# Kernel tuning notes

Measured on AMD Instinct MI355X. Metric: run time of the kernel, lower is better.

The kernel has to match this reference:

```python
import jax, jax.numpy as jnp
import numpy as np

N = 50000   # nodes
E = 800000  # edges (before self loops)
V = 30000   # vocab
D = 128     # emb_dim == hidden_dim
G = 64      # graphs in batch
L = 2       # num_layers
NEG_SLOPE = 0.2
LN_EPS = 1e-5


def setup_inputs() -> dict:
    key = jax.random.key(0)
    ks = jax.random.split(key, 12)
    node_ids = jax.random.randint(ks[0], (N,), 0, V)
    edge_index = jax.random.randint(ks[1], (2, E), 0, N)
    edge_weight = jax.random.uniform(ks[2], (E,), dtype=jnp.float32)
    batch = jnp.sort(jax.random.randint(ks[3], (N,), 0, G))
    s = 0.05
    emb = (jax.random.normal(ks[4], (V, D), dtype=jnp.float32) * s).at[0].set(0.0)  # padding_idx=0
    ln_g = jnp.ones((L, D), jnp.float32)
    ln_b = jnp.zeros((L, D), jnp.float32)
    att_w = jax.random.normal(ks[5], (L, 2 * D), dtype=jnp.float32) * s  # Linear(2D,1,bias=False)
    w1 = jax.random.normal(ks[6], (L, D, D), dtype=jnp.float32) * s
    b1 = jnp.zeros((L, D), jnp.float32)
    w2 = jax.random.normal(ks[7], (L, D, D), dtype=jnp.float32) * s
    b2 = jnp.zeros((L, D), jnp.float32)
    eps = jnp.zeros((L,), jnp.float32)  # trainable eps, init 0
    wh1 = jax.random.normal(ks[8], (D, D // 2), dtype=jnp.float32) * s
    bh1 = jnp.zeros((D // 2,), jnp.float32)
    wh2 = jax.random.normal(ks[9], (D // 2, 2), dtype=jnp.float32) * s
    bh2 = jnp.zeros((2,), jnp.float32)
    return dict(node_ids=node_ids, edge_index=edge_index, edge_weight=edge_weight, batch=batch,
                emb=emb, ln_g=ln_g, ln_b=ln_b, att_w=att_w, w1=w1, b1=b1, w2=w2, b2=b2,
                eps=eps, wh1=wh1, bh1=bh1, wh2=wh2, bh2=bh2)


def _layer_norm(x, g, b):
    mu = jnp.mean(x, axis=-1, keepdims=True)
    var = jnp.mean(jnp.square(x - mu), axis=-1, keepdims=True)
    return (x - mu) * jax.lax.rsqrt(var + LN_EPS) * g + b


def _conv(x, src, dst, ew, aw, W1, B1, W2, B2, e):
    # attention score: cat([x_i, x_j]) @ aw  ==  x_i @ aw[:D] + x_j @ aw[D:]
    score = x[dst] @ aw[:D] + x[src] @ aw[D:]            # [E2]
    score = jnp.where(score >= 0, score, NEG_SLOPE * score)  # leaky_relu(0.2)
    smax = jax.ops.segment_max(score, dst, num_segments=N)   # per-target max (all nodes have self loop)
    ex = jnp.exp(score - smax[dst])
    denom = jax.ops.segment_sum(ex, dst, num_segments=N)
    alpha = ex / (denom[dst] + 1e-16)                    # segment softmax (PyG softmax)
    alpha = alpha * ew                                   # edge weights (dropout is identity at eval)
    agg = jax.ops.segment_sum(alpha[:, None] * x[src], dst, num_segments=N)  # scatter-add messages
    out = (1.0 + e) * x + agg                            # GIN update
    return jax.nn.relu(out @ W1 + B1) @ W2 + B2          # conv MLP


def reference(node_ids, edge_index, edge_weight, batch, emb, ln_g, ln_b, att_w,
              w1, b1, w2, b2, eps, wh1, bh1, wh2, bh2):
    x = emb[node_ids]                                    # [N, D]
    loop = jnp.arange(N, dtype=edge_index.dtype)
    src = jnp.concatenate([edge_index[0], loop])         # add_self_loops
    dst = jnp.concatenate([edge_index[1], loop])
    ew = jnp.concatenate([edge_weight, jnp.ones((N,), edge_weight.dtype)])
    for l in range(L):
        x = _layer_norm(x, ln_g[l], ln_b[l])
        x = _conv(x, src, dst, ew, att_w[l], w1[l], b1[l], w2[l], b2[l], eps[l])
        x = jax.nn.relu(x)
    # global_mean_pool
    ones = jnp.ones((N,), x.dtype)
    counts = jax.ops.segment_sum(ones, batch, num_segments=G)
    g = jax.ops.segment_sum(x, batch, num_segments=G) / jnp.maximum(counts, 1.0)[:, None]
    # head MLP -> [G, 2]
    return jax.nn.relu(g @ wh1 + bh1) @ wh2 + bh2
```

## Files before the change

kernel.cpp:

```cpp
#include <hip/hip_runtime.h>

#define NN 50000
#define NPAD 50048
#define DD 128
#define GG 64
#define NBLK 49

typedef __attribute__((ext_vector_type(8))) short short8;
typedef __attribute__((ext_vector_type(4))) float f32x4;

__device__ __forceinline__ unsigned short f2bf(float f){
  union { float f; unsigned u; } x; x.f = f;
  unsigned r = x.u + 0x7fffu + ((x.u >> 16) & 1u);
  return (unsigned short)(r >> 16);
}
__device__ __forceinline__ float bf2f(unsigned short h){
  union { unsigned u; float f; } x; x.u = ((unsigned)h) << 16;
  return x.f;
}
__device__ __forceinline__ f32x4 mfma16(short8 a, short8 b, f32x4 c){
  return __builtin_amdgcn_mfma_f32_16x16x32_bf16(a, b, c, 0, 0, 0);
}

__device__ __forceinline__ float wave_reduce_sum(float v){
  #pragma unroll
  for (int off = 32; off; off >>= 1) v += __shfl_xor(v, off, 64);
  return v;
}
__device__ __forceinline__ float wave_reduce_max(float v){
  #pragma unroll
  for (int off = 32; off; off >>= 1) v = fmaxf(v, __shfl_xor(v, off, 64));
  return v;
}

__global__ __launch_bounds__(256) void gather_kernel(const int* __restrict__ ids,
    const float* __restrict__ emb, float* __restrict__ x){
  int t = blockIdx.x * 256 + threadIdx.x;
  if (t >= NN * 32) return;
  int row = t >> 5, c = (t & 31) << 2;
  int id = ids[row];
  *(float4*)&x[(size_t)row * DD + c] = *(const float4*)&emb[(size_t)id * DD + c];
}

__global__ __launch_bounds__(256) void pack_w_kernel(const float* __restrict__ w1,
    const float* __restrict__ w2, short* __restrict__ wph, short* __restrict__ wpl){
  int i = blockIdx.x * 256 + threadIdx.x;
  int m = i >> 14, k = (i >> 7) & 127, c = i & 127;
  const float* src = (m & 1) ? w2 : w1;
  float v = src[((size_t)(m >> 1) * 128 + k) * 128 + c];
  unsigned short h = f2bf(v);
  float lo = v - bf2f(h);
  int idx = (m << 14) + ((k >> 3) << 10) + (c << 3) + (k & 7);
  wph[idx] = (short)h;
  wpl[idx] = (short)f2bf(lo);
}

__global__ __launch_bounds__(256) void count_kernel(const int* __restrict__ dst,
    int* __restrict__ cnt, int E){
  int e = blockIdx.x * 256 + threadIdx.x;
  if (e < E) atomicAdd(&cnt[dst[e]], 1);
}

__global__ __launch_bounds__(256) void scan1_kernel(const int* __restrict__ cnt,
    int* __restrict__ rp, int* __restrict__ bsum){
  __shared__ int wsum[4];
  int tid = threadIdx.x, lane = tid & 63, wid = tid >> 6;
  int base = blockIdx.x * 1024 + tid * 4;
  int4 v = {0,0,0,0};
  if (base < NN) v = *(const int4*)&cnt[base];
  int tsum = v.x + v.y + v.z + v.w;
  int incl = tsum;
  #pragma unroll
  for (int off = 1; off < 64; off <<= 1){
    int t = __shfl_up(incl, off, 64);
    if (lane >= off) incl += t;
  }
  if (lane == 63) wsum[wid] = incl;
  __syncthreads();
  int woff = 0;
  for (int w = 0; w < wid; ++w) woff += wsum[w];
  int excl = woff + incl - tsum;
  if (base < NN){
    int4 o;
    o.x = excl; o.y = excl + v.x; o.z = excl + v.x + v.y; o.w = excl + v.x + v.y + v.z;
    *(int4*)&rp[base] = o;
  }
  if (tid == 0) bsum[blockIdx.x] = wsum[0] + wsum[1] + wsum[2] + wsum[3];
}

__global__ __launch_bounds__(64) void scan2_kernel(int* __restrict__ bsum, int* __restrict__ rp){
  int lane = threadIdx.x;
  int v = (lane < NBLK) ? bsum[lane] : 0;
  int incl = v;
  #pragma unroll
  for (int off = 1; off < 64; off <<= 1){
    int t = __shfl_up(incl, off, 64);
    if (lane >= off) incl += t;
  }
  if (lane < NBLK) bsum[lane] = incl - v;
  if (lane == 63) rp[NN] = incl;
}

__global__ __launch_bounds__(256) void scan3_kernel(const int* __restrict__ bsum,
    int* __restrict__ rp, int* __restrict__ cursor){
  int base = blockIdx.x * 1024 + threadIdx.x * 4;
  if (base >= NN) return;
  int add = bsum[blockIdx.x];
  int4 t = *(const int4*)&rp[base];
  t.x += add; t.y += add; t.z += add; t.w += add;
  *(int4*)&rp[base] = t;
  *(int4*)&cursor[base] = t;
}

__global__ __launch_bounds__(256) void scatter_kernel(const int* __restrict__ src,
    const int* __restrict__ dst, const float* __restrict__ ew,
    int* __restrict__ cursor, int* __restrict__ csr_src, float* __restrict__ csr_ew, int E){
  int e = blockIdx.x * 256 + threadIdx.x;
  if (e >= E) return;
  int d = dst[e];
  int p = atomicAdd(&cursor[d], 1);
  csr_src[p] = src[e];
  csr_ew[p] = ew[e];
}

__global__ __launch_bounds__(256) void ln_kernel(float* __restrict__ x,
    const float* __restrict__ gamma, const float* __restrict__ beta,
    const float* __restrict__ aw,
    float* __restrict__ sd, float* __restrict__ ss, float* __restrict__ selfsc){
  int n = (blockIdx.x * 256 + threadIdx.x) >> 6;
  int lane = threadIdx.x & 63;
  if (n >= NN) return;
  float2 v = *(const float2*)&x[(size_t)n * DD + lane * 2];
  float s  = wave_reduce_sum(v.x + v.y);
  float sq = wave_reduce_sum(v.x * v.x + v.y * v.y);
  float mu  = s * (1.0f / 128.0f);
  float var = sq * (1.0f / 128.0f) - mu * mu;
  float rs  = rsqrtf(var + 1e-5f);
  float2 g = *(const float2*)&gamma[lane * 2];
  float2 b = *(const float2*)&beta[lane * 2];
  float2 y;
  y.x = (v.x - mu) * rs * g.x + b.x;
  y.y = (v.y - mu) * rs * g.y + b.y;
  *(float2*)&x[(size_t)n * DD + lane * 2] = y;
  float2 a1 = *(const float2*)&aw[lane * 2];
  float2 a2 = *(const float2*)&aw[DD + lane * 2];
  float pd = wave_reduce_sum(y.x * a1.x + y.y * a1.y);
  float ps = wave_reduce_sum(y.x * a2.x + y.y * a2.y);
  if (lane == 0){
    sd[n] = pd; ss[n] = ps;
    float sc = pd + ps;
    selfsc[n] = sc >= 0.f ? sc : 0.2f * sc;
  }
}

__global__ __launch_bounds__(256) void wgt_kernel(
    const int* __restrict__ row_ptr, const int* __restrict__ csr_src, const float* __restrict__ csr_ew,
    const float* __restrict__ sd, const float* __restrict__ ss, const float* __restrict__ selfsc,
    const float* __restrict__ eps_arr, int layer,
    float* __restrict__ csr_w, float* __restrict__ coef){
  int n = (blockIdx.x * 256 + threadIdx.x) >> 6;
  int lane = threadIdx.x & 63;
  if (n >= NN) return;
  int beg = row_ptr[n], end = row_ptr[n + 1];
  float sdn = sd[n];
  float sf = selfsc[n];
  float m = sf;
  for (int j = beg + lane; j < end; j += 64){
    float sc = sdn + ss[csr_src[j]];
    sc = sc >= 0.f ? sc : 0.2f * sc;
    m = fmaxf(m, sc);
  }
  m = wave_reduce_max(m);
  float dsum = 0.f;
  for (int j = beg + lane; j < end; j += 64){
    float sc = sdn + ss[csr_src[j]];
    sc = sc >= 0.f ? sc : 0.2f * sc;
    dsum += expf(sc - m);
  }
  dsum = wave_reduce_sum(dsum);
  float exself = expf(sf - m);
  dsum += exself;
  float inv = 1.0f / (dsum + 1e-16f);
  for (int j = beg + lane; j < end; j += 64){
    float sc = sdn + ss[csr_src[j]];
    sc = sc >= 0.f ? sc : 0.2f * sc;
    csr_w[j] = expf(sc - m) * inv * csr_ew[j];
  }
  if (lane == 0) coef[n] = 1.0f + eps_arr[layer] + exself * inv;
}

__global__ __launch_bounds__(256) void agg2_kernel(const float* __restrict__ x,
    const int* __restrict__ row_ptr, const int* __restrict__ csr_src, const float* __restrict__ csr_w,
    const float* __restrict__ coef, short* __restrict__ aggH, short* __restrict__ aggL){
  int n = (blockIdx.x * 256 + threadIdx.x) >> 6;
  int lane = threadIdx.x & 63;
  if (n >= NN) return;
  int grp = lane >> 4, sub = lane & 15;
  int beg = row_ptr[n], end = row_ptr[n + 1];
  float4 a0 = {0,0,0,0}, a1 = {0,0,0,0};
  int j = beg + grp;
  for (; j + 4 < end; j += 8){
    int   s0 = csr_src[j];     float w0 = csr_w[j];
    int   s1 = csr_src[j + 4]; float w1 = csr_w[j + 4];
    const float4* r0 = (const float4*)&x[(size_t)s0 * DD + sub * 8];
    const float4* r1 = (const float4*)&x[(size_t)s1 * DD + sub * 8];
    float4 v00 = r0[0], v01 = r0[1];
    float4 v10 = r1[0], v11 = r1[1];
    a0.x = fmaf(w0, v00.x, a0.x); a0.y = fmaf(w0, v00.y, a0.y);
    a0.z = fmaf(w0, v00.z, a0.z); a0.w = fmaf(w0, v00.w, a0.w);
    a1.x = fmaf(w0, v01.x, a1.x); a1.y = fmaf(w0, v01.y, a1.y);
    a1.z = fmaf(w0, v01.z, a1.z); a1.w = fmaf(w0, v01.w, a1.w);
    a0.x = fmaf(w1, v10.x, a0.x); a0.y = fmaf(w1, v10.y, a0.y);
    a0.z = fmaf(w1, v10.z, a0.z); a0.w = fmaf(w1, v10.w, a0.w);
    a1.x = fmaf(w1, v11.x, a1.x); a1.y = fmaf(w1, v11.y, a1.y);
    a1.z = fmaf(w1, v11.z, a1.z); a1.w = fmaf(w1, v11.w, a1.w);
  }
  if (j < end){
    int s0 = csr_src[j]; float w0 = csr_w[j];
    const float4* r0 = (const float4*)&x[(size_t)s0 * DD + sub * 8];
    float4 v00 = r0[0], v01 = r0[1];
    a0.x = fmaf(w0, v00.x, a0.x); a0.y = fmaf(w0, v00.y, a0.y);
    a0.z = fmaf(w0, v00.z, a0.z); a0.w = fmaf(w0, v00.w, a0.w);
    a1.x = fmaf(w0, v01.x, a1.x); a1.y = fmaf(w0, v01.y, a1.y);
    a1.z = fmaf(w0, v01.z, a1.z); a1.w = fmaf(w0, v01.w, a1.w);
  }
  #pragma unroll
  for (int mask = 16; mask <= 32; mask <<= 1){
    a0.x += __shfl_xor(a0.x, mask, 64); a0.y += __shfl_xor(a0.y, mask, 64);
    a0.z += __shfl_xor(a0.z, mask, 64); a0.w += __shfl_xor(a0.w, mask, 64);
    a1.x += __shfl_xor(a1.x, mask, 64); a1.y += __shfl_xor(a1.y, mask, 64);
    a1.z += __shfl_xor(a1.z, mask, 64); a1.w += __shfl_xor(a1.w, mask, 64);
  }
  if (grp == 0){
    float c = coef[n];
    const float4* xr = (const float4*)&x[(size_t)n * DD + sub * 8];
    float4 x0 = xr[0], x1 = xr[1];
    float vv[8];
    vv[0] = fmaf(c, x0.x, a0.x); vv[1] = fmaf(c, x0.y, a0.y);
    vv[2] = fmaf(c, x0.z, a0.z); vv[3] = fmaf(c, x0.w, a0.w);
    vv[4] = fmaf(c, x1.x, a1.x); vv[5] = fmaf(c, x1.y, a1.y);
    vv[6] = fmaf(c, x1.z, a1.z); vv[7] = fmaf(c, x1.w, a1.w);
    short8 H, L;
    #pragma unroll
    for (int i = 0; i < 8; ++i){
      unsigned short h = f2bf(vv[i]);
      H[i] = (short)h;
      L[i] = (short)f2bf(vv[i] - bf2f(h));
    }
    *(short8*)&aggH[(size_t)n * DD + sub * 8] = H;
    *(short8*)&aggL[(size_t)n * DD + sub * 8] = L;
  }
}

template<int MODE>
__global__ __launch_bounds__(256) void mlp_mfma_kernel(
    const short* __restrict__ aH, const short* __restrict__ aL,
    const short* __restrict__ w1h, const short* __restrict__ w1l,
    const short* __restrict__ w2h, const short* __restrict__ w2l,
    const float* __restrict__ B1, const float* __restrict__ B2,
    const float* __restrict__ g2, const float* __restrict__ be2,
    const float* __restrict__ aw2,
    float* __restrict__ xout, float* __restrict__ sd, float* __restrict__ ss,
    float* __restrict__ selfsc){
  __shared__ __align__(16) short hh[64 * DD];
  __shared__ __align__(16) short hl[64 * DD];
  int tid = threadIdx.x;
  int w = tid >> 6, l = tid & 63;
  int g = l >> 4, c16 = l & 15;
  int base = blockIdx.x * 64;
  int rowA = base + w * 16 + c16;

  short8 a1h[4], a1l[4];
  #pragma unroll
  for (int ks = 0; ks < 4; ++ks){
    size_t off = (size_t)rowA * DD + ks * 32 + g * 8;
    a1h[ks] = *(const short8*)(aH + off);
    a1l[ks] = *(const short8*)(aL + off);
  }

  f32x4 acc[8];
  #pragma unroll
  for (int ct = 0; ct < 8; ++ct){
    f32x4 a = {0.f, 0.f, 0.f, 0.f};
    #pragma unroll
    for (int ks = 0; ks < 4; ++ks){
      int bo = (((ks * 4 + g) * 128) + ct * 16 + c16) * 8;
      short8 bh = *(const short8*)(w1h + bo);
      short8 bl = *(const short8*)(w1l + bo);
      a = mfma16(a1h[ks], bh, a);
      a = mfma16(a1l[ks], bh, a);
      a = mfma16(a1h[ks], bl, a);
    }
    acc[ct] = a;
  }

  #pragma unroll
  for (int ct = 0; ct < 8; ++ct){
    int col = ct * 16 + c16;
    float b = B1[col];
    #pragma unroll
    for (int r = 0; r < 4; ++r){
      int rl = w * 16 + g * 4 + r;
      float v = acc[ct][r] + b;
      v = v > 0.f ? v : 0.f;
      unsigned short h = f2bf(v);
      int idx = rl * DD + ((((col >> 3) ^ (rl & 7))) << 3) + (col & 7);
      hh[idx] = (short)h;
      hl[idx] = (short)f2bf(v - bf2f(h));
    }
  }
  __syncthreads();

  int rowL = w * 16 + c16;
  short8 a2h[4], a2l[4];
  #pragma unroll
  for (int ks = 0; ks < 4; ++ks){
    int chunk = ks * 4 + g;
    int idx = rowL * DD + ((chunk ^ (rowL & 7)) << 3);
    a2h[ks] = *(const short8*)&hh[idx];
    a2l[ks] = *(const short8*)&hl[idx];
  }

  #pragma unroll
  for (int ct = 0; ct < 8; ++ct){
    f32x4 a = {0.f, 0.f, 0.f, 0.f};
    #pragma unroll
    for (int ks = 0; ks < 4; ++ks){
      int bo = (((ks * 4 + g) * 128) + ct * 16 + c16) * 8;
      short8 bh = *(const short8*)(w2h + bo);
      short8 bl = *(const short8*)(w2l + bo);
      a = mfma16(a2h[ks], bh, a);
      a = mfma16(a2l[ks], bh, a);
      a = mfma16(a2h[ks], bl, a);
    }
    acc[ct] = a;
  }

  #pragma unroll
  for (int ct = 0; ct < 8; ++ct){
    int col = ct * 16 + c16;
    float b = B2[col];
    #pragma unroll
    for (int r = 0; r < 4; ++r){
      float v = acc[ct][r] + b;
      acc[ct][r] = v > 0.f ? v : 0.f;
    }
  }

  if (MODE == 1){
    #pragma unroll
    for (int ct = 0; ct < 8; ++ct){
      int col = ct * 16 + c16;
      #pragma unroll
      for (int r = 0; r < 4; ++r){
        int row = base + w * 16 + g * 4 + r;
        if (row < NN) xout[(size_t)row * DD + col] = acc[ct][r];
      }
    }
  } else {
    float s[4] = {0,0,0,0}, sq[4] = {0,0,0,0};
    #pragma unroll
    for (int ct = 0; ct < 8; ++ct)
      #pragma unroll
      for (int r = 0; r < 4; ++r){ float v = acc[ct][r]; s[r] += v; sq[r] += v * v; }
    #pragma unroll
    for (int off = 1; off < 16; off <<= 1){
      #pragma unroll
      for (int r = 0; r < 4; ++r){
        s[r]  += __shfl_xor(s[r],  off, 64);
        sq[r] += __shfl_xor(sq[r], off, 64);
      }
    }
    float mu[4], rs[4];
    #pragma unroll
    for (int r = 0; r < 4; ++r){
      mu[r] = s[r] * (1.f / 128.f);
      float var = sq[r] * (1.f / 128.f) - mu[r] * mu[r];
      rs[r] = rsqrtf(var + 1e-5f);
    }
    float pd[4] = {0,0,0,0}, ps[4] = {0,0,0,0};
    #pragma unroll
    for (int ct = 0; ct < 8; ++ct){
      int col = ct * 16 + c16;
      float gam = g2[col], bet = be2[col];
      float aa = aw2[col], ab = aw2[DD + col];
      #pragma unroll
      for (int r = 0; r < 4; ++r){
        float y = (acc[ct][r] - mu[r]) * rs[r] * gam + bet;
        acc[ct][r] = y;
        pd[r] += y * aa; ps[r] += y * ab;
      }
    }
    #pragma unroll
    for (int off = 1; off < 16; off <<= 1){
      #pragma unroll
      for (int r = 0; r < 4; ++r){
        pd[r] += __shfl_xor(pd[r], off, 64);
        ps[r] += __shfl_xor(ps[r], off, 64);
      }
    }
    #pragma unroll
    for (int ct = 0; ct < 8; ++ct){
      int col = ct * 16 + c16;
      #pragma unroll
      for (int r = 0; r < 4; ++r){
        int row = base + w * 16 + g * 4 + r;
        if (row < NN) xout[(size_t)row * DD + col] = acc[ct][r];
      }
    }
    if (c16 == 0){
      #pragma unroll
      for (int r = 0; r < 4; ++r){
        int row = base + w * 16 + g * 4 + r;
        if (row < NN){
          sd[row] = pd[r]; ss[row] = ps[r];
          float sc = pd[r] + ps[r];
          selfsc[row] = sc >= 0.f ? sc : 0.2f * sc;
        }
      }
    }
  }
}

__global__ __launch_bounds__(128) void pool_kernel(const float* __restrict__ x,
    const int* __restrict__ batch, float* __restrict__ gsum, int* __restrict__ gcnt){
  int g = blockIdx.x >> 2, part = blockIdx.x & 3;
  int lo = 0, hi = NN;
  while (lo < hi){ int mid = (lo + hi) >> 1; if (batch[mid] < g) lo = mid + 1; else hi = mid; }
  int beg = lo;
  lo = beg; hi = NN;
  while (lo < hi){ int mid = (lo + hi) >> 1; if (batch[mid] < g + 1) lo = mid + 1; else hi = mid; }
  int end = lo;
  int cg = end - beg;
  int rb = beg + (int)((long long)cg * part / 4);
  int re = beg + (int)((long long)cg * (part + 1) / 4);
  int d = threadIdx.x;
  float sum = 0.f;
  for (int r = rb; r < re; ++r) sum += x[(size_t)r * DD + d];
  atomicAdd(&gsum[g * DD + d], sum);
  if (d == 0 && part == 0) gcnt[g] = cg;
}

__global__ __launch_bounds__(256) void head_kernel(const float* __restrict__ gsum,
    const int* __restrict__ gcnt,
    const float* __restrict__ wh1, const float* __restrict__ bh1,
    const float* __restrict__ wh2, const float* __restrict__ bh2,
    float* __restrict__ outp){
  __shared__ float gm[GG * DD];
  __shared__ float h[GG * 64];
  int tid = threadIdx.x;
  for (int i = tid; i < GG * DD; i += 256){
    int g = i >> 7;
    int c = gcnt[g];
    gm[i] = gsum[i] / (float)(c > 0 ? c : 1);
  }
  __syncthreads();
  for (int i = tid; i < GG * 64; i += 256){
    int r = i >> 6, c = i & 63;
    float a0 = 0.f, a1 = 0.f;
    for (int k = 0; k < DD; k += 2){
      a0 = fmaf(gm[r * DD + k],     wh1[k * 64 + c],       a0);
      a1 = fmaf(gm[r * DD + k + 1], wh1[(k + 1) * 64 + c], a1);
    }
    float v = a0 + a1 + bh1[c];
    h[i] = v > 0.f ? v : 0.f;
  }
  __syncthreads();
  if (tid < GG * 2){
    int r = tid >> 1, c = tid & 1;
    float a = 0.f;
    for (int k = 0; k < 64; ++k) a = fmaf(h[r * 64 + k], wh2[k * 2 + c], a);
    outp[tid] = a + bh2[c];
  }
}

extern "C" void kernel_launch(void* const* d_in, const int* in_sizes, int n_in,
                              void* d_out, int out_size, void* d_ws, size_t ws_size,
                              hipStream_t stream){
  const int*   node_ids    = (const int*)  d_in[0];
  const int*   edge_index  = (const int*)  d_in[1];
  const float* edge_weight = (const float*)d_in[2];
  const int*   batch       = (const int*)  d_in[3];
  const float* emb         = (const float*)d_in[4];
  const float* ln_g        = (const float*)d_in[5];
  const float* ln_b        = (const float*)d_in[6];
  const float* att_w       = (const float*)d_in[7];
  const float* w1          = (const float*)d_in[8];
  const float* b1          = (const float*)d_in[9];
  const float* w2          = (const float*)d_in[10];
  const float* b2          = (const float*)d_in[11];
  const float* eps         = (const float*)d_in[12];
  const float* wh1         = (const float*)d_in[13];
  const float* bh1         = (const float*)d_in[14];
  const float* wh2         = (const float*)d_in[15];
  const float* bh2         = (const float*)d_in[16];
  int E = in_sizes[1] / 2;
  const int* srcp = edge_index;
  const int* dstp = edge_index + E;

  char* w = (char*)d_ws;
  float* x       = (float*)w; w += (size_t)NN * DD * 4;
  short* aggH    = (short*)w; w += (size_t)NPAD * DD * 2;
  short* aggL    = (short*)w; w += (size_t)NPAD * DD * 2;
  short* wph     = (short*)w; w += (size_t)4 * 16384 * 2;
  short* wpl     = (short*)w; w += (size_t)4 * 16384 * 2;
  float* sd      = (float*)w; w += (size_t)NN * 4;
  float* ssb     = (float*)w; w += (size_t)NN * 4;
  float* selfsc  = (float*)w; w += (size_t)NN * 4;
  float* coef    = (float*)w; w += (size_t)NN * 4;
  int*   cnt     = (int*)  w; w += (size_t)NN * 4;
  int*   row_ptr = (int*)  w; w += (size_t)(NN + 8) * 4;
  int*   cursor  = (int*)  w; w += (size_t)NN * 4;
  int*   bsum    = (int*)  w; w += (size_t)64 * 4;
  int*   csr_src = (int*)  w; w += (size_t)E * 4;
  float* csr_ew  = (float*)w; w += (size_t)E * 4;
  float* csr_w   = (float*)w; w += (size_t)E * 4;
  float* gsum    = (float*)w; w += (size_t)GG * DD * 4;
  int*   gcnt    = (int*)  w; w += (size_t)GG * 4;

  hipMemsetAsync(cnt, 0, (size_t)NN * 4, stream);
  hipMemsetAsync(gsum, 0, (size_t)GG * DD * 4, stream);

  count_kernel<<<(E + 255) / 256, 256, 0, stream>>>(dstp, cnt, E);
  scan1_kernel<<<NBLK, 256, 0, stream>>>(cnt, row_ptr, bsum);
  scan2_kernel<<<1, 64, 0, stream>>>(bsum, row_ptr);
  scan3_kernel<<<NBLK, 256, 0, stream>>>(bsum, row_ptr, cursor);
  scatter_kernel<<<(E + 255) / 256, 256, 0, stream>>>(srcp, dstp, edge_weight, cursor, csr_src, csr_ew, E);
  gather_kernel<<<(NN * 32 + 255) / 256, 256, 0, stream>>>(node_ids, emb, x);
  pack_w_kernel<<<256, 256, 0, stream>>>(w1, w2, wph, wpl);

  ln_kernel<<<(NN + 3) / 4, 256, 0, stream>>>(x, ln_g, ln_b, att_w, sd, ssb, selfsc);

  int mlp_grid = (NN + 63) / 64;
  wgt_kernel <<<(NN + 3) / 4, 256, 0, stream>>>(row_ptr, csr_src, csr_ew,
                                                sd, ssb, selfsc, eps, 0, csr_w, coef);
  agg2_kernel<<<(NN + 3) / 4, 256, 0, stream>>>(x, row_ptr, csr_src, csr_w, coef, aggH, aggL);
  mlp_mfma_kernel<0><<<mlp_grid, 256, 0, stream>>>(aggH, aggL,
      wph, wpl, wph + 16384, wpl + 16384, b1, b2,
      ln_g + DD, ln_b + DD, att_w + 2 * DD, x, sd, ssb, selfsc);
  wgt_kernel <<<(NN + 3) / 4, 256, 0, stream>>>(row_ptr, csr_src, csr_ew,
                                                sd, ssb, selfsc, eps, 1, csr_w, coef);
  agg2_kernel<<<(NN + 3) / 4, 256, 0, stream>>>(x, row_ptr, csr_src, csr_w, coef, aggH, aggL);
  mlp_mfma_kernel<1><<<mlp_grid, 256, 0, stream>>>(aggH, aggL,
      wph + 2 * 16384, wpl + 2 * 16384, wph + 3 * 16384, wpl + 3 * 16384,
      b1 + DD, b2 + DD, ln_g + DD, ln_b + DD, att_w + 2 * DD, x, sd, ssb, selfsc);

  pool_kernel<<<GG * 4, 128, 0, stream>>>(x, batch, gsum, gcnt);
  head_kernel<<<1, 256, 0, stream>>>(gsum, gcnt, wh1, bh1, wh2, bh2, (float*)d_out);
}
```

Baseline: 511.9 us.

## Gather neighbor features in bf16, fuse embedding gather with layernorm, widen pooling

Keeps a bf16 copy of node features, written by the layernorm and MLP epilogues, and has the edge aggregation read that copy instead of fp32 rows. This halves the bytes moved by the irregular neighbor gather, the main memory-bound stage. The embedding gather is fused into the first layernorm kernel, removing one full pass over x. Pooling also gets four times more blocks and an unrolled accumulation loop. The cost is lower precision in the aggregated messages and extra bf16 stores from the MLP epilogue.

```diff
diff --git a/kernel.cpp b/kernel.cpp
--- a/kernel.cpp
+++ b/kernel.cpp
@@ -7,6 +7,7 @@
 #define NBLK 49
 
 typedef __attribute__((ext_vector_type(8))) short short8;
+typedef __attribute__((ext_vector_type(8))) unsigned short ushort8;
 typedef __attribute__((ext_vector_type(4))) float f32x4;
 
 __device__ __forceinline__ unsigned short f2bf(float f){
@@ -33,13 +34,39 @@
   return v;
 }
 
-__global__ __launch_bounds__(256) void gather_kernel(const int* __restrict__ ids,
-    const float* __restrict__ emb, float* __restrict__ x){
-  int t = blockIdx.x * 256 + threadIdx.x;
-  if (t >= NN * 32) return;
-  int row = t >> 5, c = (t & 31) << 2;
-  int id = ids[row];
-  *(float4*)&x[(size_t)row * DD + c] = *(const float4*)&emb[(size_t)id * DD + c];
+__global__ __launch_bounds__(256) void gather_ln_kernel(const int* __restrict__ ids,
+    const float* __restrict__ emb,
+    const float* __restrict__ gamma, const float* __restrict__ beta,
+    const float* __restrict__ aw,
+    float* __restrict__ x, unsigned short* __restrict__ xbf,
+    float* __restrict__ sd, float* __restrict__ ss, float* __restrict__ selfsc){
+  int n = (blockIdx.x * 256 + threadIdx.x) >> 6;
+  int lane = threadIdx.x & 63;
+  if (n >= NN) return;
+  int id = ids[n];
+  float2 v = *(const float2*)&emb[(size_t)id * DD + lane * 2];
+  float s  = wave_reduce_sum(v.x + v.y);
+  float sq = wave_reduce_sum(v.x * v.x + v.y * v.y);
+  float mu  = s * (1.0f / 128.0f);
+  float var = sq * (1.0f / 128.0f) - mu * mu;
+  float rs  = rsqrtf(var + 1e-5f);
+  float2 g = *(const float2*)&gamma[lane * 2];
+  float2 b = *(const float2*)&beta[lane * 2];
+  float2 y;
+  y.x = (v.x - mu) * rs * g.x + b.x;
+  y.y = (v.y - mu) * rs * g.y + b.y;
+  *(float2*)&x[(size_t)n * DD + lane * 2] = y;
+  unsigned pk = (unsigned)f2bf(y.x) | ((unsigned)f2bf(y.y) << 16);
+  ((unsigned*)xbf)[(size_t)n * 64 + lane] = pk;
+  float2 a1 = *(const float2*)&aw[lane * 2];
+  float2 a2 = *(const float2*)&aw[DD + lane * 2];
+  float pd = wave_reduce_sum(y.x * a1.x + y.y * a1.y);
+  float ps = wave_reduce_sum(y.x * a2.x + y.y * a2.y);
+  if (lane == 0){
+    sd[n] = pd; ss[n] = ps;
+    float sc = pd + ps;
+    selfsc[n] = sc >= 0.f ? sc : 0.2f * sc;
+  }
 }
 
 __global__ __launch_bounds__(256) void pack_w_kernel(const float* __restrict__ w1,
@@ -121,36 +148,6 @@
   int p = atomicAdd(&cursor[d], 1);
   csr_src[p] = src[e];
   csr_ew[p] = ew[e];
-}
-
-__global__ __launch_bounds__(256) void ln_kernel(float* __restrict__ x,
-    const float* __restrict__ gamma, const float* __restrict__ beta,
-    const float* __restrict__ aw,
-    float* __restrict__ sd, float* __restrict__ ss, float* __restrict__ selfsc){
-  int n = (blockIdx.x * 256 + threadIdx.x) >> 6;
-  int lane = threadIdx.x & 63;
-  if (n >= NN) return;
-  float2 v = *(const float2*)&x[(size_t)n * DD + lane * 2];
-  float s  = wave_reduce_sum(v.x + v.y);
-  float sq = wave_reduce_sum(v.x * v.x + v.y * v.y);
-  float mu  = s * (1.0f / 128.0f);
-  float var = sq * (1.0f / 128.0f) - mu * mu;
-  float rs  = rsqrtf(var + 1e-5f);
-  float2 g = *(const float2*)&gamma[lane * 2];
-  float2 b = *(const float2*)&beta[lane * 2];
-  float2 y;
-  y.x = (v.x - mu) * rs * g.x + b.x;
-  y.y = (v.y - mu) * rs * g.y + b.y;
-  *(float2*)&x[(size_t)n * DD + lane * 2] = y;
-  float2 a1 = *(const float2*)&aw[lane * 2];
-  float2 a2 = *(const float2*)&aw[DD + lane * 2];
-  float pd = wave_reduce_sum(y.x * a1.x + y.y * a1.y);
-  float ps = wave_reduce_sum(y.x * a2.x + y.y * a2.y);
-  if (lane == 0){
-    sd[n] = pd; ss[n] = ps;
-    float sc = pd + ps;
-    selfsc[n] = sc >= 0.f ? sc : 0.2f * sc;
-  }
 }
 
 __global__ __launch_bounds__(256) void wgt_kernel(
@@ -190,6 +187,7 @@
 }
 
 __global__ __launch_bounds__(256) void agg2_kernel(const float* __restrict__ x,
+    const unsigned short* __restrict__ xbf,
     const int* __restrict__ row_ptr, const int* __restrict__ csr_src, const float* __restrict__ csr_w,
     const float* __restrict__ coef, short* __restrict__ aggH, short* __restrict__ aggL){
   int n = (blockIdx.x * 256 + threadIdx.x) >> 6;
@@ -197,55 +195,43 @@
   if (n >= NN) return;
   int grp = lane >> 4, sub = lane & 15;
   int beg = row_ptr[n], end = row_ptr[n + 1];
-  float4 a0 = {0,0,0,0}, a1 = {0,0,0,0};
+  float a[8] = {0,0,0,0,0,0,0,0};
   int j = beg + grp;
   for (; j + 4 < end; j += 8){
     int   s0 = csr_src[j];     float w0 = csr_w[j];
     int   s1 = csr_src[j + 4]; float w1 = csr_w[j + 4];
-    const float4* r0 = (const float4*)&x[(size_t)s0 * DD + sub * 8];
-    const float4* r1 = (const float4*)&x[(size_t)s1 * DD + sub * 8];
-    float4 v00 = r0[0], v01 = r0[1];
-    float4 v10 = r1[0], v11 = r1[1];
-    a0.x = fmaf(w0, v00.x, a0.x); a0.y = fmaf(w0, v00.y, a0.y);
-    a0.z = fmaf(w0, v00.z, a0.z); a0.w = fmaf(w0, v00.w, a0.w);
-    a1.x = fmaf(w0, v01.x, a1.x); a1.y = fmaf(w0, v01.y, a1.y);
-    a1.z = fmaf(w0, v01.z, a1.z); a1.w = fmaf(w0, v01.w, a1.w);
-    a0.x = fmaf(w1, v10.x, a0.x); a0.y = fmaf(w1, v10.y, a0.y);
-    a0.z = fmaf(w1, v10.z, a0.z); a0.w = fmaf(w1, v10.w, a0.w);
-    a1.x = fmaf(w1, v11.x, a1.x); a1.y = fmaf(w1, v11.y, a1.y);
-    a1.z = fmaf(w1, v11.z, a1.z); a1.w = fmaf(w1, v11.w, a1.w);
+    ushort8 u0 = *(const ushort8*)&xbf[(size_t)s0 * DD + sub * 8];
+    ushort8 u1 = *(const ushort8*)&xbf[(size_t)s1 * DD + sub * 8];
+    #pragma unroll
+    for (int i = 0; i < 8; ++i) a[i] = fmaf(w0, bf2f(u0[i]), a[i]);
+    #pragma unroll
+    for (int i = 0; i < 8; ++i) a[i] = fmaf(w1, bf2f(u1[i]), a[i]);
   }
   if (j < end){
     int s0 = csr_src[j]; float w0 = csr_w[j];
-    const float4* r0 = (const float4*)&x[(size_t)s0 * DD + sub * 8];
-    float4 v00 = r0[0], v01 = r0[1];
-    a0.x = fmaf(w0, v00.x, a0.x); a0.y = fmaf(w0, v00.y, a0.y);
-    a0.z = fmaf(w0, v00.z, a0.z); a0.w = fmaf(w0, v00.w, a0.w);
-    a1.x = fmaf(w0, v01.x, a1.x); a1.y = fmaf(w0, v01.y, a1.y);
-    a1.z = fmaf(w0, v01.z, a1.z); a1.w = fmaf(w0, v01.w, a1.w);
+    ushort8 u0 = *(const ushort8*)&xbf[(size_t)s0 * DD + sub * 8];
+    #pragma unroll
+    for (int i = 0; i < 8; ++i) a[i] = fmaf(w0, bf2f(u0[i]), a[i]);
   }
   #pragma unroll
   for (int mask = 16; mask <= 32; mask <<= 1){
-    a0.x += __shfl_xor(a0.x, mask, 64); a0.y += __shfl_xor(a0.y, mask, 64);
-    a0.z += __shfl_xor(a0.z, mask, 64); a0.w += __shfl_xor(a0.w, mask, 64);
-    a1.x += __shfl_xor(a1.x, mask, 64); a1.y += __shfl_xor(a1.y, mask, 64);
-    a1.z += __shfl_xor(a1.z, mask, 64); a1.w += __shfl_xor(a1.w, mask, 64);
+    #pragma unroll
+    for (int i = 0; i < 8; ++i) a[i] += __shfl_xor(a[i], mask, 64);
   }
   if (grp == 0){
     float c = coef[n];
     const float4* xr = (const float4*)&x[(size_t)n * DD + sub * 8];
     float4 x0 = xr[0], x1 = xr[1];
-    float vv[8];
-    vv[0] = fmaf(c, x0.x, a0.x); vv[1] = fmaf(c, x0.y, a0.y);
-    vv[2] = fmaf(c, x0.z, a0.z); vv[3] = fmaf(c, x0.w, a0.w);
-    vv[4] = fmaf(c, x1.x, a1.x); vv[5] = fmaf(c, x1.y, a1.y);
-    vv[6] = fmaf(c, x1.z, a1.z); vv[7] = fmaf(c, x1.w, a1.w);
+    a[0] = fmaf(c, x0.x, a[0]); a[1] = fmaf(c, x0.y, a[1]);
+    a[2] = fmaf(c, x0.z, a[2]); a[3] = fmaf(c, x0.w, a[3]);
+    a[4] = fmaf(c, x1.x, a[4]); a[5] = fmaf(c, x1.y, a[5]);
+    a[6] = fmaf(c, x1.z, a[6]); a[7] = fmaf(c, x1.w, a[7]);
     short8 H, L;
     #pragma unroll
     for (int i = 0; i < 8; ++i){
-      unsigned short h = f2bf(vv[i]);
+      unsigned short h = f2bf(a[i]);
       H[i] = (short)h;
-      L[i] = (short)f2bf(vv[i] - bf2f(h));
+      L[i] = (short)f2bf(a[i] - bf2f(h));
     }
     *(short8*)&aggH[(size_t)n * DD + sub * 8] = H;
     *(short8*)&aggL[(size_t)n * DD + sub * 8] = L;
@@ -260,7 +246,8 @@
     const float* __restrict__ B1, const float* __restrict__ B2,
     const float* __restrict__ g2, const float* __restrict__ be2,
     const float* __restrict__ aw2,
-    float* __restrict__ xout, float* __restrict__ sd, float* __restrict__ ss,
+    float* __restrict__ xout, unsigned short* __restrict__ xbf,
+    float* __restrict__ sd, float* __restrict__ ss,
     float* __restrict__ selfsc){
   __shared__ __align__(16) short hh[64 * DD];
   __shared__ __align__(16) short hl[64 * DD];
@@ -405,7 +392,11 @@
       #pragma unroll
       for (int r = 0; r < 4; ++r){
         int row = base + w * 16 + g * 4 + r;
-        if (row < NN) xout[(size_t)row * DD + col] = acc[ct][r];
+        if (row < NN){
+          float y = acc[ct][r];
+          xout[(size_t)row * DD + col] = y;
+          xbf[(size_t)row * DD + col] = f2bf(y);
+        }
       }
     }
     if (c16 == 0){
@@ -424,7 +415,7 @@
 
 __global__ __launch_bounds__(128) void pool_kernel(const float* __restrict__ x,
     const int* __restrict__ batch, float* __restrict__ gsum, int* __restrict__ gcnt){
-  int g = blockIdx.x >> 2, part = blockIdx.x & 3;
+  int g = blockIdx.x >> 4, part = blockIdx.x & 15;
   int lo = 0, hi = NN;
   while (lo < hi){ int mid = (lo + hi) >> 1; if (batch[mid] < g) lo = mid + 1; else hi = mid; }
   int beg = lo;
@@ -432,11 +423,19 @@
   while (lo < hi){ int mid = (lo + hi) >> 1; if (batch[mid] < g + 1) lo = mid + 1; else hi = mid; }
   int end = lo;
   int cg = end - beg;
-  int rb = beg + (int)((long long)cg * part / 4);
-  int re = beg + (int)((long long)cg * (part + 1) / 4);
+  int rb = beg + (int)((long long)cg * part / 16);
+  int re = beg + (int)((long long)cg * (part + 1) / 16);
   int d = threadIdx.x;
-  float sum = 0.f;
-  for (int r = rb; r < re; ++r) sum += x[(size_t)r * DD + d];
+  float s0 = 0.f, s1 = 0.f, s2 = 0.f, s3 = 0.f;
+  int r = rb;
+  for (; r + 3 < re; r += 4){
+    s0 += x[(size_t)r * DD + d];
+    s1 += x[(size_t)(r + 1) * DD + d];
+    s2 += x[(size_t)(r + 2) * DD + d];
+    s3 += x[(size_t)(r + 3) * DD + d];
+  }
+  for (; r < re; ++r) s0 += x[(size_t)r * DD + d];
+  float sum = (s0 + s1) + (s2 + s3);
   atomicAdd(&gsum[g * DD + d], sum);
   if (d == 0 && part == 0) gcnt[g] = cg;
 }
@@ -500,6 +499,7 @@
 
   char* w = (char*)d_ws;
   float* x       = (float*)w; w += (size_t)NN * DD * 4;
+  unsigned short* xbf = (unsigned short*)w; w += (size_t)NN * DD * 2;
   short* aggH    = (short*)w; w += (size_t)NPAD * DD * 2;
   short* aggL    = (short*)w; w += (size_t)NPAD * DD * 2;
   short* wph     = (short*)w; w += (size_t)4 * 16384 * 2;
@@ -526,25 +526,24 @@
   scan2_kernel<<<1, 64, 0, stream>>>(bsum, row_ptr);
   scan3_kernel<<<NBLK, 256, 0, stream>>>(bsum, row_ptr, cursor);
   scatter_kernel<<<(E + 255) / 256, 256, 0, stream>>>(srcp, dstp, edge_weight, cursor, csr_src, csr_ew, E);
-  gather_kernel<<<(NN * 32 + 255) / 256, 256, 0, stream>>>(node_ids, emb, x);
   pack_w_kernel<<<256, 256, 0, stream>>>(w1, w2, wph, wpl);
-
-  ln_kernel<<<(NN + 3) / 4, 256, 0, stream>>>(x, ln_g, ln_b, att_w, sd, ssb, selfsc);
+  gather_ln_kernel<<<(NN + 3) / 4, 256, 0, stream>>>(node_ids, emb, ln_g, ln_b, att_w,
+                                                     x, xbf, sd, ssb, selfsc);
 
   int mlp_grid = (NN + 63) / 64;
   wgt_kernel <<<(NN + 3) / 4, 256, 0, stream>>>(row_ptr, csr_src, csr_ew,
                                                 sd, ssb, selfsc, eps, 0, csr_w, coef);
-  agg2_kernel<<<(NN + 3) / 4, 256, 0, stream>>>(x, row_ptr, csr_src, csr_w, coef, aggH, aggL);
+  agg2_kernel<<<(NN + 3) / 4, 256, 0, stream>>>(x, xbf, row_ptr, csr_src, csr_w, coef, aggH, aggL);
   mlp_mfma_kernel<0><<<mlp_grid, 256, 0, stream>>>(aggH, aggL,
       wph, wpl, wph + 16384, wpl + 16384, b1, b2,
-      ln_g + DD, ln_b + DD, att_w + 2 * DD, x, sd, ssb, selfsc);
+      ln_g + DD, ln_b + DD, att_w + 2 * DD, x, xbf, sd, ssb, selfsc);
   wgt_kernel <<<(NN + 3) / 4, 256, 0, stream>>>(row_ptr, csr_src, csr_ew,
                                                 sd, ssb, selfsc, eps, 1, csr_w, coef);
-  agg2_kernel<<<(NN + 3) / 4, 256, 0, stream>>>(x, row_ptr, csr_src, csr_w, coef, aggH, aggL);
+  agg2_kernel<<<(NN + 3) / 4, 256, 0, stream>>>(x, xbf, row_ptr, csr_src, csr_w, coef, aggH, aggL);
   mlp_mfma_kernel<1><<<mlp_grid, 256, 0, stream>>>(aggH, aggL,
       wph + 2 * 16384, wpl + 2 * 16384, wph + 3 * 16384, wpl + 3 * 16384,
-      b1 + DD, b2 + DD, ln_g + DD, ln_b + DD, att_w + 2 * DD, x, sd, ssb, selfsc);
-
-  pool_kernel<<<GG * 4, 128, 0, stream>>>(x, batch, gsum, gcnt);
+      b1 + DD, b2 + DD, ln_g + DD, ln_b + DD, att_w + 2 * DD, x, xbf, sd, ssb, selfsc);
+
+  pool_kernel<<<GG * 16, 128, 0, stream>>>(x, batch, gsum, gcnt);
   head_kernel<<<1, 256, 0, stream>>>(gsum, gcnt, wh1, bh1, wh2, bh2, (float*)d_out);
 }
```

Measured after the change: 425.7 us. -16.8%, faster.
